# Performance work log

Hardware: AMD Instinct MI355X
Metric: run time of the kernel (lower is better)

The kernel has to match this reference:

```python
import jax, jax.numpy as jnp
import numpy as np

DIM = 24
HID = 256
N = 4096
NUM_LO = DIM * (DIM - 1) // 2  # 276
NEG = -0.01  # slope used in the hand-written Jacobians (source uses -0.01, NOT the fwd leaky slope 0.01; faithful)


def _linear_params(key, out_dim, in_dim):
    kw, kb = jax.random.split(key)
    s = 1.0 / np.sqrt(in_dim)
    W = jax.random.uniform(kw, (out_dim, in_dim), jnp.float32, -s, s)
    b = jax.random.uniform(kb, (out_dim,), jnp.float32, -s, s)
    return W, b


def setup_inputs() -> dict:
    key = jax.random.key(0)
    k = jax.random.split(key, 7)
    W1, b1 = _linear_params(k[0], HID, DIM)
    W2, b2 = _linear_params(k[1], HID, HID)
    WG, bG = _linear_params(k[2], DIM, HID)
    WLd, bLd = _linear_params(k[3], DIM, HID)
    WLo, bLo = _linear_params(k[4], NUM_LO, HID)
    q = jax.random.normal(k[5], (N, DIM), jnp.float32)
    q_dot = jax.random.normal(k[6], (N, DIM), jnp.float32)
    return {"q": q, "q_dot": q_dot, "W1": W1, "b1": b1, "W2": W2, "b2": b2,
            "WG": WG, "bG": bG, "WLd": WLd, "bLd": bLd, "WLo": WLo, "bLo": bLo}


def _forward(q, q_dot, W1, b1, W2, b2, WG, bG, WLd, bLd, WLo, bLo):
    n, d = q.shape
    tr, tc = np.tril_indices(d, -1)  # row-major strict-lower order == torch mask-flatten order
    di = np.arange(d)
    # MLP trunk (torch leaky_relu default slope 0.01)
    h1 = jax.nn.leaky_relu(q @ W1.T + b1)                       # [n,HID]
    h2 = jax.nn.leaky_relu(h1 @ W2.T + b2)                      # [n,HID]
    h3 = h2 @ WLd.T + bLd                                       # [n,d]
    g = h2 @ WG.T + bG                                          # [n,d]
    Ld = jax.nn.softplus(h3)                                    # [n,d]
    Lo = h2 @ WLo.T + bLo                                       # [n,NUM_LO]
    # Lower-triangular L (diag_embed(Ld) + masked strict-lower fill)
    L = jnp.zeros((n, d, d), q.dtype).at[:, tr, tc].set(Lo).at[:, di, di].set(Ld)
    # Hand-written Jacobian chain; diag_embed(v)@W == v[:,:,None]*W (direct elementwise scaling)
    dR1 = jnp.where(h1 > 0, 1.0, NEG)
    J1 = dR1[:, :, None] * W1                                    # dh1/dq  [n,HID,d]
    dR2 = jnp.where(h2 > 0, 1.0, NEG)
    J2 = dR2[:, :, None] * jnp.einsum('ij,njd->nid', W2, J1)     # dh2/dq  [n,HID,d]
    sig = jax.nn.sigmoid(h3)
    dld_dq = sig[:, :, None] * jnp.einsum('ij,njd->nid', WLd, J2)  # [n,d,d]
    dlo_dq = jnp.einsum('oj,njd->nod', WLo, J2)                  # [n,NUM_LO,d]
    dld_dt = jnp.einsum('nid,nd->ni', dld_dq, q_dot)             # [n,d]
    dlo_dt = jnp.einsum('nod,nd->no', dlo_dq, q_dot)             # [n,NUM_LO]
    dL_dt = jnp.zeros((n, d, d), q.dtype).at[:, tr, tc].set(dlo_dt).at[:, di, di].set(dld_dt)
    # 4D assembly: torch does L[L==1] = dlo_dq.view(-1), which reinterprets the (lo, q_idx)
    # flat buffer in (q_idx, tril_pos) order -> plain reshape replicates that exactly.
    vals = dlo_dq.reshape(n, d, NUM_LO)
    dld_dq_p = dld_dq.transpose(0, 2, 1)                         # [n, d_q, d_ld]
    dL_dq = jnp.zeros((n, d, d, d), q.dtype).at[:, :, tr, tc].set(vals).at[:, :, di, di].set(dld_dq_p)
    eye = jnp.eye(d, dtype=q.dtype)
    M = L @ L.transpose(0, 2, 1) + 1e-9 * eye
    dM_dt = L @ dL_dt.transpose(0, 2, 1) + dL_dt @ L.transpose(0, 2, 1)
    # Quadratic term. torch: q_dot.repeat(d,1)/L.repeat(d,1,1) index as (i % n) while
    # dL_dq.view(n*d,d,d) indexes as (i // d, i % d) -> replicate exactly (faithful).
    idx = jnp.arange(n * d) % n
    qd_r = q_dot[idx]                                            # [n*d, d]
    L_r = L[idx]                                                 # [n*d, d, d]
    dL_i = dL_dq.reshape(n * d, d, d)
    S = dL_i @ L_r.transpose(0, 2, 1) + L_r @ dL_i.transpose(0, 2, 1)
    quad = jnp.einsum('bi,bij,bj->b', qd_r, S, qd_r).reshape(n, d)
    c = jnp.einsum('nij,nj->ni', dM_dt, q_dot) - 0.5 * quad
    return M, c, g


def reference(q, q_dot, W1, b1, W2, b2, WG, bG, WLd, bLd, WLo, bLo):
    return _forward(q, q_dot, W1, b1, W2, b2, WG, bG, WLd, bLd, WLo, bLo)
```

## Files before the change

### kernel.cpp

```cpp
#include <hip/hip_runtime.h>
#include <math.h>

#define DIM 24
#define HID 256
#define NLO 276
#define NSAMP 4096
#define C_OFF 2359296
#define G_OFF 2457600

#define OFF_W2FH 0
#define OFF_W2FL 32768
#define OFF_WEFH 65536
#define OFF_WEFL 106496
#define OFF_W1H16 147456
#define OFF_W1L16 151552
#define OFF_W2H16 155648
#define OFF_W2L16 188416
#define OFF_WHH16 221184
#define OFF_WHL16 264192
#define OFF_MSKT 307200
#define OFF_SIGT 372736
#define OFF_LDT  471040
#define OFF_UT   569344
#define OFF_LOT  667648
#define OFF_W1PH 1798144
#define OFF_W1PL 1801216
#define OFF_W1NH 1804288
#define OFF_W1NL 1807360

typedef __attribute__((ext_vector_type(8))) short bf16x8;
typedef __attribute__((ext_vector_type(8))) _Float16 f16x8;
typedef __attribute__((ext_vector_type(4))) float f32x4;

__device__ __forceinline__ float leaky(float x){ return x > 0.f ? x : 0.01f*x; }
__device__ __forceinline__ unsigned short f2b(float f){
  unsigned u = __float_as_uint(f);
  return (unsigned short)((u + 0x7FFFu + ((u >> 16) & 1u)) >> 16);
}
__device__ __forceinline__ float b2f(unsigned short h){ return __uint_as_float(((unsigned)h) << 16); }
__device__ __forceinline__ void f2h2(float v, unsigned short* hi, unsigned short* lo){
  _Float16 h = (_Float16)v;
  _Float16 l = (_Float16)((v - (float)h) * 4096.f);
  *hi = *(unsigned short*)&h; *lo = *(unsigned short*)&l;
}

__global__ __launch_bounds__(256) void k0_prep(
    const float* __restrict__ W1, const float* __restrict__ W2,
    const float* __restrict__ WG, const float* __restrict__ WLd,
    const float* __restrict__ WLo, float* __restrict__ ws)
{
  const int tid = blockIdx.x*256 + threadIdx.x;
  const int nth = gridDim.x*256;
  unsigned short* W2FH = (unsigned short*)(ws + OFF_W2FH);
  unsigned short* W2FL = (unsigned short*)(ws + OFF_W2FL);
  for (int e = tid; e < 65536; e += nth){
    int j=e&7, l=(e>>3)&63, kb=(e>>9)&7, mt=e>>12;
    int m = mt*16+(l&15), k = kb*32+((l>>4)&3)*8+j;
    float v = W2[m*256+k];
    unsigned short h = f2b(v);
    W2FH[e]=h; W2FL[e]=f2b(v-b2f(h));
  }
  unsigned short* WEFH = (unsigned short*)(ws + OFF_WEFH);
  unsigned short* WEFL = (unsigned short*)(ws + OFF_WEFL);
  for (int e = tid; e < 81920; e += nth){
    int j=e&7, l=(e>>3)&63, kb=(e>>9)&7, mt=e>>12;
    int r = mt*16+(l&15), k = kb*32+((l>>4)&3)*8+j;
    float v = 0.f;
    if (r < 24) v = WLd[r*256+k]; else if (r < 300) v = WLo[(r-24)*256+k];
    unsigned short h = f2b(v);
    WEFH[e]=h; WEFL[e]=f2b(v-b2f(h));
  }
  unsigned short* W1H = (unsigned short*)(ws + OFF_W1H16);
  unsigned short* W1L = (unsigned short*)(ws + OFF_W1L16);
  for (int e = tid; e < 8192; e += nth){
    int j=e&7, l=(e>>3)&63, mt=e>>9;
    int m = mt*16+(l&15), k = ((l>>4)&3)*8+j;
    float v = (k < 24) ? W1[m*24+k] : 0.f;
    f2h2(v, &W1H[e], &W1L[e]);
  }
  unsigned short* W2H = (unsigned short*)(ws + OFF_W2H16);
  unsigned short* W2L = (unsigned short*)(ws + OFF_W2L16);
  for (int e = tid; e < 65536; e += nth){
    int j=e&7, l=(e>>3)&63, kb=(e>>9)&7, mt=e>>12;
    int m = mt*16+(l&15), k = kb*32+((l>>4)&3)*8+j;
    f2h2(W2[m*256+k], &W2H[e], &W2L[e]);
  }
  unsigned short* WHH = (unsigned short*)(ws + OFF_WHH16);
  unsigned short* WHL = (unsigned short*)(ws + OFF_WHL16);
  for (int e = tid; e < 86016; e += nth){
    int j=e&7, l=(e>>3)&63, kb=(e>>9)&7, mt=e>>12;
    int rr = mt*16+(l&15), k = kb*32+((l>>4)&3)*8+j;
    float v = 0.f;
    if (rr < 24) v = WLd[rr*256+k];
    else if (rr < 48) v = WG[(rr-24)*256+k];
    else if (rr < 324) v = WLo[(rr-48)*256+k];
    f2h2(v, &WHH[e], &WHL[e]);
  }
  unsigned short* W1PH = (unsigned short*)(ws + OFF_W1PH);
  unsigned short* W1PL = (unsigned short*)(ws + OFF_W1PL);
  unsigned short* W1NH = (unsigned short*)(ws + OFF_W1NH);
  unsigned short* W1NL = (unsigned short*)(ws + OFF_W1NL);
  for (int e = tid; e < 6144; e += nth){
    float v = W1[e];
    unsigned short h = f2b(v);
    W1PH[e] = h; W1PL[e] = f2b(v - b2f(h));
    float vn = -0.01f*v;
    unsigned short hn = f2b(vn);
    W1NH[e] = hn; W1NL[e] = f2b(vn - b2f(hn));
  }
}

__global__ __launch_bounds__(256) void k1_fwd(
    const float* __restrict__ q, const float* __restrict__ qd_g,
    const float* __restrict__ b1, const float* __restrict__ b2,
    const float* __restrict__ bG, const float* __restrict__ bLd,
    const float* __restrict__ bLo, float* __restrict__ ws,
    float* __restrict__ out)
{
  const int s0 = blockIdx.x*8, t = threadIdx.x;
  const int w = t>>6, l = t&63, l15 = l&15, l4g = (l>>4)&3;
  unsigned* MSKT = (unsigned*)(ws + OFF_MSKT);
  float* SIGT = ws + OFF_SIGT;
  float* LDT  = ws + OFF_LDT;
  float* UT   = ws + OFF_UT;
  float* LOT  = ws + OFF_LOT;

  __shared__ __align__(16) unsigned short pool[8448];
  __shared__ unsigned char mb[8][64];
  __shared__ float qd_s[8][24];
  __shared__ float Lsm[8][600];
  unsigned short* BQH = pool;
  unsigned short* BQL = BQH + 320;
  unsigned short* BH2 = pool;
  unsigned short* BL2 = BH2 + 2112;

  for (int f = t; f < 192; f += 256){
    float v = q[s0*24 + f];
    int n = f/24, k = f%24;
    f2h2(v, &BQH[n*40+k], &BQL[n*40+k]);
    ((float*)qd_s)[f] = qd_g[s0*24 + f];
  }
  if (t < 64){ int n = t>>3, k = 24 + (t&7); BQH[n*40+k]=0; BQL[n*40+k]=0; }
  __syncthreads();

  f32x4 aH[4], aX[4];
  #pragma unroll
  for (int i=0;i<4;++i){ aH[i]=(f32x4){0,0,0,0}; aX[i]=(f32x4){0,0,0,0}; }
  {
    const f16x8* WH = (const f16x8*)(ws + OFF_W1H16);
    const f16x8* WL = (const f16x8*)(ws + OFF_W1L16);
    f16x8 Af[4], Al[4];
    #pragma unroll
    for (int i=0;i<4;++i){ int mt=w+4*i; Af[i]=WH[mt*64+l]; Al[i]=WL[mt*64+l]; }
    int off = l15*40 + l4g*8;
    f16x8 Bh = *(const f16x8*)(BQH+off), Bl = *(const f16x8*)(BQL+off);
    #pragma unroll
    for (int i=0;i<4;++i){
      aH[i]=__builtin_amdgcn_mfma_f32_16x16x32_f16(Af[i],Bh,aH[i],0,0,0);
      aX[i]=__builtin_amdgcn_mfma_f32_16x16x32_f16(Af[i],Bl,aX[i],0,0,0);
      aX[i]=__builtin_amdgcn_mfma_f32_16x16x32_f16(Al[i],Bh,aX[i],0,0,0);
    }
  }
  __syncthreads();
  #pragma unroll
  for (int i=0;i<4;++i){
    int m0=(w+4*i)*16+4*l4g;
    float4 bb = *(const float4*)(b1+m0);
    int n = l15;
    if (n < 8){
      unsigned nib=0; unsigned short hs[4], ls[4];
      #pragma unroll
      for (int r=0;r<4;++r){
        float val = aH[i][r] + aX[i][r]*(1.f/4096.f) + ((const float*)&bb)[r];
        if (val > 0.f) nib |= 1u<<r;
        f2h2(leaky(val), &hs[r], &ls[r]);
      }
      mb[n][(m0>>2)] = (unsigned char)nib;
      *(uint2*)(BH2 + n*264 + m0) = make_uint2((unsigned)hs[0]|((unsigned)hs[1]<<16),
                                               (unsigned)hs[2]|((unsigned)hs[3]<<16));
      *(uint2*)(BL2 + n*264 + m0) = make_uint2((unsigned)ls[0]|((unsigned)ls[1]<<16),
                                               (unsigned)ls[2]|((unsigned)ls[3]<<16));
    }
  }
  __syncthreads();
  if (t < 64){
    int n = t&7, w8 = t>>3; unsigned word = 0;
    #pragma unroll
    for (int b=0;b<8;++b) word |= (unsigned)(mb[n][w8*8+b] & 0xFu) << (4*b);
    MSKT[w8*NSAMP + s0+n] = word;
  }

  #pragma unroll
  for (int i=0;i<4;++i){ aH[i]=(f32x4){0,0,0,0}; aX[i]=(f32x4){0,0,0,0}; }
  {
    const f16x8* WH = (const f16x8*)(ws + OFF_W2H16);
    const f16x8* WL = (const f16x8*)(ws + OFF_W2L16);
    for (int kb=0;kb<8;++kb){
      f16x8 Af[4], Al[4];
      #pragma unroll
      for (int i=0;i<4;++i){ int mt=w+4*i; Af[i]=WH[(mt*8+kb)*64+l]; Al[i]=WL[(mt*8+kb)*64+l]; }
      int off = l15*264 + kb*32 + l4g*8;
      f16x8 Bh = *(const f16x8*)(BH2+off), Bl = *(const f16x8*)(BL2+off);
      #pragma unroll
      for (int i=0;i<4;++i){
        aH[i]=__builtin_amdgcn_mfma_f32_16x16x32_f16(Af[i],Bh,aH[i],0,0,0);
        aX[i]=__builtin_amdgcn_mfma_f32_16x16x32_f16(Af[i],Bl,aX[i],0,0,0);
        aX[i]=__builtin_amdgcn_mfma_f32_16x16x32_f16(Al[i],Bh,aX[i],0,0,0);
      }
    }
  }
  __syncthreads();
  #pragma unroll
  for (int i=0;i<4;++i){
    int m0=(w+4*i)*16+4*l4g;
    float4 bb = *(const float4*)(b2+m0);
    int n = l15;
    if (n < 8){
      unsigned nib=0; unsigned short hs[4], ls[4];
      #pragma unroll
      for (int r=0;r<4;++r){
        float val = aH[i][r] + aX[i][r]*(1.f/4096.f) + ((const float*)&bb)[r];
        if (val > 0.f) nib |= 1u<<r;
        f2h2(leaky(val), &hs[r], &ls[r]);
      }
      mb[n][(m0>>2)] = (unsigned char)nib;
      *(uint2*)(BH2 + n*264 + m0) = make_uint2((unsigned)hs[0]|((unsigned)hs[1]<<16),
                                               (unsigned)hs[2]|((unsigned)hs[3]<<16));
      *(uint2*)(BL2 + n*264 + m0) = make_uint2((unsigned)ls[0]|((unsigned)ls[1]<<16),
                                               (unsigned)ls[2]|((unsigned)ls[3]<<16));
    }
  }
  __syncthreads();
  if (t < 64){
    int n = t&7, w8 = t>>3; unsigned word = 0;
    #pragma unroll
    for (int b=0;b<8;++b) word |= (unsigned)(mb[n][w8*8+b] & 0xFu) << (4*b);
    MSKT[(8+w8)*NSAMP + s0+n] = word;
  }

  for (int pass=0; pass<2; ++pass){
    f32x4 cH[3], cX[3];
    #pragma unroll
    for (int i=0;i<3;++i){ cH[i]=(f32x4){0,0,0,0}; cX[i]=(f32x4){0,0,0,0}; }
    const f16x8* WH = (const f16x8*)(ws + OFF_WHH16);
    const f16x8* WL = (const f16x8*)(ws + OFF_WHL16);
    for (int kb=0;kb<8;++kb){
      f16x8 Af[3], Al[3];
      #pragma unroll
      for (int i=0;i<3;++i){
        int mt = w + 4*(3*pass+i);
        if (mt < 21){ Af[i]=WH[(mt*8+kb)*64+l]; Al[i]=WL[(mt*8+kb)*64+l]; }
      }
      int off = l15*264 + kb*32 + l4g*8;
      f16x8 Bh = *(const f16x8*)(BH2+off), Bl = *(const f16x8*)(BL2+off);
      #pragma unroll
      for (int i=0;i<3;++i){
        int mt = w + 4*(3*pass+i);
        if (mt < 21){
          cH[i]=__builtin_amdgcn_mfma_f32_16x16x32_f16(Af[i],Bh,cH[i],0,0,0);
          cX[i]=__builtin_amdgcn_mfma_f32_16x16x32_f16(Af[i],Bl,cX[i],0,0,0);
          cX[i]=__builtin_amdgcn_mfma_f32_16x16x32_f16(Al[i],Bh,cX[i],0,0,0);
        }
      }
    }
    #pragma unroll
    for (int i=0;i<3;++i){
      int mt = w + 4*(3*pass+i);
      if (mt >= 21) continue;
      int m0 = mt*16+4*l4g;
      int n = l15;
      if (n < 8){
        int sG = s0+n;
        int tr = 0, tc = 0;
        if (m0 >= 48){
          int p = m0 - 48;
          tr = (int)((1.f + sqrtf(1.f + 8.f*(float)p))*0.5f);
          while (tr*(tr-1)/2 > p) --tr;
          while ((tr+1)*tr/2 <= p) ++tr;
          tc = p - tr*(tr-1)/2;
        }
        #pragma unroll
        for (int r=0;r<4;++r){
          int rr = m0+r;
          float val = cH[i][r] + cX[i][r]*(1.f/4096.f);
          if (rr < 24){
            val += bLd[rr];
            SIGT[rr*NSAMP + sG] = 1.f/(1.f + expf(-val));
            float sp = fmaxf(val,0.f) + log1pf(expf(-fabsf(val)));
            LDT[rr*NSAMP + sG] = sp;
            Lsm[n][rr*25 + rr] = sp;
          } else if (rr < 48){
            out[G_OFF + sG*24 + (rr-24)] = val + bG[rr-24];
          } else if (rr < 324){
            float lov = val + bLo[rr-48];
            LOT[(rr-48)*NSAMP + sG] = lov;
            Lsm[n][tr*25 + tc] = lov;
            if (++tc == tr){ ++tr; tc = 0; }
          }
        }
      }
    }
  }
  __syncthreads();

  for (int n2 = 0; n2 < 8; ++n2){
    const float* Ls = Lsm[n2];
    for (int e = t; e < 576; e += 256){
      int r = e/24, c = e%24, km = min(r,c);
      float acc = (r == c) ? 1e-9f : 0.f;
      for (int k = 0; k <= km; ++k) acc += Ls[r*25+k]*Ls[c*25+k];
      out[(size_t)(s0+n2)*576 + e] = acc;
    }
  }
  if (t < 192){
    int n = t/24, c = t%24;
    float u = qd_s[n][c]*Lsm[n][c*25+c];
    for (int r = c+1; r < 24; ++r) u += qd_s[n][r]*Lsm[n][r*25+c];
    UT[c*NSAMP + s0+n] = u;
  }
}

__global__ __launch_bounds__(256, 3) void kDE(
    const float* __restrict__ q_dot, float* __restrict__ ws, float* __restrict__ out)
{
  const int n0 = blockIdx.x*2, t = threadIdx.x;
  const int w = t >> 6, l = t & 63;
  const int l15 = l & 15, l4g = (l >> 4) & 3;
  const unsigned* MSKT = (const unsigned*)(ws + OFF_MSKT);
  const float* SIGT = ws + OFF_SIGT;
  const float* LDT  = ws + OFF_LDT;
  const float* UT   = ws + OFF_UT;
  const float* LOT  = ws + OFF_LOT;

  __shared__ __align__(16) char pool[50688];
  __shared__ unsigned msk[2][16];
  unsigned short* BH = (unsigned short*)pool;
  unsigned short* BL = BH + 12672;
  float* dlo_flat = (float*)pool;
  float* dld25    = (float*)(pool + 26496);
  float* qdm_s    = (float*)(pool + 28896);
  float* um_s     = (float*)(pool + 31296);
  float* qp2      = (float*)(pool + 33696);
  float* dtlo     = (float*)(pool + 40320);
  float* dtld     = (float*)(pool + 41424);
  float* w1s      = (float*)(pool + 41520);
  float* sigs     = (float*)(pool + 41616);
  float* qds      = (float*)(pool + 41712);
  float* uss      = (float*)(pool + 41808);
  float* qps      = (float*)(pool + 41904);

  if (t < 32) msk[t>>4][t&15] = MSKT[(t&15)*NSAMP + n0 + (t>>4)];
  __syncthreads();

  {
    bool p0 = (msk[0][t>>5] >> (t&31)) & 1u;
    bool p1 = (msk[1][t>>5] >> (t&31)) & 1u;
    const unsigned* h0 = (const unsigned*)((const unsigned short*)(ws + (p0 ? OFF_W1PH : OFF_W1NH)) + t*24);
    const unsigned* l0 = (const unsigned*)((const unsigned short*)(ws + (p0 ? OFF_W1PL : OFF_W1NL)) + t*24);
    const unsigned* h1 = (const unsigned*)((const unsigned short*)(ws + (p1 ? OFF_W1PH : OFF_W1NH)) + t*24);
    const unsigned* l1 = (const unsigned*)((const unsigned short*)(ws + (p1 ? OFF_W1PL : OFF_W1NL)) + t*24);
    #pragma unroll
    for (int j = 0; j < 12; ++j){
      unsigned dh0 = h0[j], dl0 = l0[j], dh1 = h1[j], dl1 = l1[j];
      BH[(2*j)*264 + t]      = (unsigned short)dh0;
      BH[(2*j+1)*264 + t]    = (unsigned short)(dh0 >> 16);
      BL[(2*j)*264 + t]      = (unsigned short)dl0;
      BL[(2*j+1)*264 + t]    = (unsigned short)(dl0 >> 16);
      BH[(24+2*j)*264 + t]   = (unsigned short)dh1;
      BH[(24+2*j+1)*264 + t] = (unsigned short)(dh1 >> 16);
      BL[(24+2*j)*264 + t]   = (unsigned short)dl1;
      BL[(24+2*j+1)*264 + t] = (unsigned short)(dl1 >> 16);
    }
  }
  __syncthreads();

  f32x4 accD[4][3];
  #pragma unroll
  for (int i = 0; i < 4; ++i)
    #pragma unroll
    for (int nt = 0; nt < 3; ++nt) accD[i][nt] = (f32x4){0.f,0.f,0.f,0.f};
  {
    const bf16x8* AHp = (const bf16x8*)(ws + OFF_W2FH);
    const bf16x8* ALp = (const bf16x8*)(ws + OFF_W2FL);
    for (int kb = 0; kb < 8; ++kb){
      bf16x8 AH[4], AL[4], BHf[3], BLf[3];
      #pragma unroll
      for (int i = 0; i < 4; ++i){
        int mt = 4*w + i;
        AH[i] = AHp[(mt*8+kb)*64 + l];
        AL[i] = ALp[(mt*8+kb)*64 + l];
      }
      #pragma unroll
      for (int nt = 0; nt < 3; ++nt){
        int off = (nt*16 + l15)*264 + kb*32 + l4g*8;
        BHf[nt] = *(const bf16x8*)(BH + off);
        BLf[nt] = *(const bf16x8*)(BL + off);
      }
      #pragma unroll
      for (int i = 0; i < 4; ++i)
        #pragma unroll
        for (int nt = 0; nt < 3; ++nt){
          accD[i][nt] = __builtin_amdgcn_mfma_f32_16x16x32_bf16(AH[i], BHf[nt], accD[i][nt], 0, 0, 0);
          accD[i][nt] = __builtin_amdgcn_mfma_f32_16x16x32_bf16(AH[i], BLf[nt], accD[i][nt], 0, 0, 0);
          accD[i][nt] = __builtin_amdgcn_mfma_f32_16x16x32_bf16(AL[i], BHf[nt], accD[i][nt], 0, 0, 0);
        }
    }
  }
  __syncthreads();

  #pragma unroll
  for (int i = 0; i < 4; ++i){
    int mt = 4*w + i;
    int m0 = mt*16 + 4*l4g;
    int bb = m0 & 31;
    #pragma unroll
    for (int nt = 0; nt < 3; ++nt){
      int c = nt*16 + l15;
      int s = c >= 24;
      unsigned word = msk[s][8 + (mt>>1)];
      unsigned uh[4], ul[4];
      #pragma unroll
      for (int r = 0; r < 4; ++r){
        float sc = ((word >> (bb + r)) & 1u) ? 1.f : -0.01f;
        float v = sc * accD[i][nt][r];
        unsigned uv = __float_as_uint(v);
        uh[r] = uv;
        float lo = v - __uint_as_float(uv & 0xFFFF0000u);
        ul[r] = __float_as_uint(lo);
      }
      *(uint2*)(BH + c*264 + m0) = make_uint2((uh[0]>>16) | (uh[1] & 0xFFFF0000u),
                                              (uh[2]>>16) | (uh[3] & 0xFFFF0000u));
      *(uint2*)(BL + c*264 + m0) = make_uint2((ul[0]>>16) | (ul[1] & 0xFFFF0000u),
                                              (ul[2]>>16) | (ul[3] & 0xFFFF0000u));
    }
  }
  __syncthreads();

  f32x4 accE[5][3];
  #pragma unroll
  for (int i = 0; i < 5; ++i)
    #pragma unroll
    for (int nt = 0; nt < 3; ++nt) accE[i][nt] = (f32x4){0.f,0.f,0.f,0.f};
  {
    const bf16x8* AHp = (const bf16x8*)(ws + OFF_WEFH);
    const bf16x8* ALp = (const bf16x8*)(ws + OFF_WEFL);
    for (int kb = 0; kb < 8; ++kb){
      bf16x8 AH[5], AL[5], BHf[3], BLf[3];
      #pragma unroll
      for (int i = 0; i < 5; ++i){
        int mt = 5*w + i;
        AH[i] = AHp[(mt*8+kb)*64 + l];
        AL[i] = ALp[(mt*8+kb)*64 + l];
      }
      #pragma unroll
      for (int nt = 0; nt < 3; ++nt){
        int off = (nt*16 + l15)*264 + kb*32 + l4g*8;
        BHf[nt] = *(const bf16x8*)(BH + off);
        BLf[nt] = *(const bf16x8*)(BL + off);
      }
      #pragma unroll
      for (int i = 0; i < 5; ++i)
        #pragma unroll
        for (int nt = 0; nt < 3; ++nt){
          accE[i][nt] = __builtin_amdgcn_mfma_f32_16x16x32_bf16(AH[i], BHf[nt], accE[i][nt], 0, 0, 0);
          accE[i][nt] = __builtin_amdgcn_mfma_f32_16x16x32_bf16(AH[i], BLf[nt], accE[i][nt], 0, 0, 0);
          accE[i][nt] = __builtin_amdgcn_mfma_f32_16x16x32_bf16(AL[i], BHf[nt], accE[i][nt], 0, 0, 0);
        }
    }
  }
  __syncthreads();

  for (int s = 0; s < 2; ++s){
    const int n = n0 + s;
    #pragma unroll
    for (int i = 0; i < 5; ++i){
      int mt = 5*w + i;
      #pragma unroll
      for (int nt = 0; nt < 3; ++nt){
        int c = nt*16 + l15;
        if ((c >= 24) == (s == 1)){
          int d = c - 24*s;
          #pragma unroll
          for (int r = 0; r < 4; ++r){
            int re = mt*16 + 4*l4g + r;
            if (re < 24) dld25[re*25 + d] = accE[i][nt][r];
            else if (re < 300) dlo_flat[(re-24)*24 + d] = accE[i][nt][r];
          }
        }
      }
    }
    for (int e = t; e < 576; e += 256){
      int a_ = e/24, b_ = e%24;
      int ma = (n*24 + a_) & (NSAMP-1);
      int mb_ = (n*24 + b_) & (NSAMP-1);
      qdm_s[a_*25 + b_] = q_dot[ma*24 + b_];
      um_s[a_*25 + b_]  = UT[a_*NSAMP + mb_];
    }
    if (t < 24){
      sigs[t] = SIGT[t*NSAMP + n];
      qds[t]  = q_dot[n*24 + t];
      uss[t]  = UT[t*NSAMP + n];
    }
    __syncthreads();

    for (int k = t; k < 1656; k += 256){
      float4 v = *(const float4*)(dlo_flat + 4*k);
      int j4 = (k % 6)*4;
      qp2[k] = v.x*qds[j4] + v.y*qds[j4+1] + v.z*qds[j4+2] + v.w*qds[j4+3];
    }
    if (t < 24){
      float a = 0.f;
      #pragma unroll
      for (int d = 0; d < 24; ++d) a += dld25[t*25+d]*qds[d];
      dtld[t] = sigs[t]*a;
    }
    __syncthreads();

    for (int o = t; o < 276; o += 256){
      float a = 0.f;
      #pragma unroll
      for (int j = 0; j < 6; ++j) a += qp2[o*6+j];
      dtlo[o] = a;
    }
    __syncthreads();

    if (t < 96){
      int g = t/24, i = t%24;
      float part = 0.f;
      for (int c2 = g; c2 < 24; c2 += 4){
        float v = qdm_s[i*25+c2]*sigs[c2]*dld25[c2*25+i];
        for (int r = c2+1; r < 24; ++r){
          int p = r*(r-1)/2 + c2;
          v += qdm_s[i*25+r]*dlo_flat[i*276 + p];
        }
        part += um_s[c2*25+i]*v;
      }
      qps[g*24 + i] = part;
    } else if (t >= 128 && t < 152){
      int i = t - 128;
      float a = qds[i]*dtld[i];
      for (int j = i+1; j < 24; ++j) a += qds[j]*dtlo[j*(j-1)/2 + i];
      w1s[i] = a;
    }
    __syncthreads();

    if (t < 24){
      const int i = t;
      float cs = dtld[i]*uss[i] + LDT[i*NSAMP + n]*w1s[i];
      for (int k = 0; k < i; ++k){
        int p = i*(i-1)/2 + k;
        cs += LOT[p*NSAMP + n]*w1s[k] + dtlo[p]*uss[k];
      }
      float quad = qps[i] + qps[24+i] + qps[48+i] + qps[72+i];
      out[C_OFF + n*24 + i] = cs - quad;
    }
    __syncthreads();
  }
}

extern "C" void kernel_launch(void* const* d_in, const int* in_sizes, int n_in,
                              void* d_out, int out_size, void* d_ws, size_t ws_size,
                              hipStream_t stream)
{
  const float* q   = (const float*)d_in[0];
  const float* qd  = (const float*)d_in[1];
  const float* W1  = (const float*)d_in[2];
  const float* b1  = (const float*)d_in[3];
  const float* W2  = (const float*)d_in[4];
  const float* b2  = (const float*)d_in[5];
  const float* WG  = (const float*)d_in[6];
  const float* bG  = (const float*)d_in[7];
  const float* WLd = (const float*)d_in[8];
  const float* bLd = (const float*)d_in[9];
  const float* WLo = (const float*)d_in[10];
  const float* bLo = (const float*)d_in[11];
  float* out = (float*)d_out;
  float* ws  = (float*)d_ws;

  k0_prep<<<256, 256, 0, stream>>>(W1, W2, WG, WLd, WLo, ws);
  k1_fwd<<<NSAMP/8, 256, 0, stream>>>(q, qd, b1, b2, bG, bLd, bLo, ws, out);
  kDE<<<NSAMP/2, 256, 0, stream>>>(qd, ws, out);
}
```

Measured before the change: 254.4 us.

## Halve samples per forward block and build W1 Jacobian tiles on the fly

The forward kernel now handles 4 samples per block instead of 8 and launches twice as many blocks, so more CUs have work during the MLP stage. Each MFMA tile is 16 columns wide, so fewer of its columns now carry real samples and weights are reloaded per block more often. The prep kernel no longer precomputes sign-scaled bf16 hi/lo copies of W1. Instead the Jacobian kernel reads W1 directly, scales it by the activation-slope mask and splits it into bf16 hi/lo in registers. This drops a workspace pass but adds conversion arithmetic to every Jacobian block.

```diff
diff --git a/kernel.cpp b/kernel.cpp
--- a/kernel.cpp
+++ b/kernel.cpp
@@ -23,10 +23,6 @@
 #define OFF_LDT  471040
 #define OFF_UT   569344
 #define OFF_LOT  667648
-#define OFF_W1PH 1798144
-#define OFF_W1PL 1801216
-#define OFF_W1NH 1804288
-#define OFF_W1NL 1807360
 
 typedef __attribute__((ext_vector_type(8))) short bf16x8;
 typedef __attribute__((ext_vector_type(8))) _Float16 f16x8;
@@ -96,18 +92,6 @@
     else if (rr < 324) v = WLo[(rr-48)*256+k];
     f2h2(v, &WHH[e], &WHL[e]);
   }
-  unsigned short* W1PH = (unsigned short*)(ws + OFF_W1PH);
-  unsigned short* W1PL = (unsigned short*)(ws + OFF_W1PL);
-  unsigned short* W1NH = (unsigned short*)(ws + OFF_W1NH);
-  unsigned short* W1NL = (unsigned short*)(ws + OFF_W1NL);
-  for (int e = tid; e < 6144; e += nth){
-    float v = W1[e];
-    unsigned short h = f2b(v);
-    W1PH[e] = h; W1PL[e] = f2b(v - b2f(h));
-    float vn = -0.01f*v;
-    unsigned short hn = f2b(vn);
-    W1NH[e] = hn; W1NL[e] = f2b(vn - b2f(hn));
-  }
 }
 
 __global__ __launch_bounds__(256) void k1_fwd(
@@ -117,7 +101,7 @@
     const float* __restrict__ bLo, float* __restrict__ ws,
     float* __restrict__ out)
 {
-  const int s0 = blockIdx.x*8, t = threadIdx.x;
+  const int s0 = blockIdx.x*4, t = threadIdx.x;
   const int w = t>>6, l = t&63, l15 = l&15, l4g = (l>>4)&3;
   unsigned* MSKT = (unsigned*)(ws + OFF_MSKT);
   float* SIGT = ws + OFF_SIGT;
@@ -126,21 +110,21 @@
   float* LOT  = ws + OFF_LOT;
 
   __shared__ __align__(16) unsigned short pool[8448];
-  __shared__ unsigned char mb[8][64];
-  __shared__ float qd_s[8][24];
-  __shared__ float Lsm[8][600];
+  __shared__ unsigned char mb[4][64];
+  __shared__ float qd_s[4][24];
+  __shared__ float Lsm[4][600];
   unsigned short* BQH = pool;
-  unsigned short* BQL = BQH + 320;
+  unsigned short* BQL = BQH + 160;
   unsigned short* BH2 = pool;
-  unsigned short* BL2 = BH2 + 2112;
-
-  for (int f = t; f < 192; f += 256){
+  unsigned short* BL2 = BH2 + 4224;
+
+  for (int f = t; f < 96; f += 256){
     float v = q[s0*24 + f];
     int n = f/24, k = f%24;
     f2h2(v, &BQH[n*40+k], &BQL[n*40+k]);
     ((float*)qd_s)[f] = qd_g[s0*24 + f];
   }
-  if (t < 64){ int n = t>>3, k = 24 + (t&7); BQH[n*40+k]=0; BQL[n*40+k]=0; }
+  if (t < 32){ int n = t>>3, k = 24 + (t&7); BQH[n*40+k]=0; BQL[n*40+k]=0; }
   __syncthreads();
 
   f32x4 aH[4], aX[4];
@@ -167,7 +151,7 @@
     int m0=(w+4*i)*16+4*l4g;
     float4 bb = *(const float4*)(b1+m0);
     int n = l15;
-    if (n < 8){
+    if (n < 4){
       unsigned nib=0; unsigned short hs[4], ls[4];
       #pragma unroll
       for (int r=0;r<4;++r){
@@ -183,8 +167,8 @@
     }
   }
   __syncthreads();
-  if (t < 64){
-    int n = t&7, w8 = t>>3; unsigned word = 0;
+  if (t < 32){
+    int n = t&3, w8 = t>>2; unsigned word = 0;
     #pragma unroll
     for (int b=0;b<8;++b) word |= (unsigned)(mb[n][w8*8+b] & 0xFu) << (4*b);
     MSKT[w8*NSAMP + s0+n] = word;
@@ -215,7 +199,7 @@
     int m0=(w+4*i)*16+4*l4g;
     float4 bb = *(const float4*)(b2+m0);
     int n = l15;
-    if (n < 8){
+    if (n < 4){
       unsigned nib=0; unsigned short hs[4], ls[4];
       #pragma unroll
       for (int r=0;r<4;++r){
@@ -231,8 +215,8 @@
     }
   }
   __syncthreads();
-  if (t < 64){
-    int n = t&7, w8 = t>>3; unsigned word = 0;
+  if (t < 32){
+    int n = t&3, w8 = t>>2; unsigned word = 0;
     #pragma unroll
     for (int b=0;b<8;++b) word |= (unsigned)(mb[n][w8*8+b] & 0xFu) << (4*b);
     MSKT[(8+w8)*NSAMP + s0+n] = word;
@@ -269,7 +253,7 @@
       if (mt >= 21) continue;
       int m0 = mt*16+4*l4g;
       int n = l15;
-      if (n < 8){
+      if (n < 4){
         int sG = s0+n;
         int tr = 0, tc = 0;
         if (m0 >= 48){
@@ -303,7 +287,7 @@
   }
   __syncthreads();
 
-  for (int n2 = 0; n2 < 8; ++n2){
+  for (int n2 = 0; n2 < 4; ++n2){
     const float* Ls = Lsm[n2];
     for (int e = t; e < 576; e += 256){
       int r = e/24, c = e%24, km = min(r,c);
@@ -312,7 +296,7 @@
       out[(size_t)(s0+n2)*576 + e] = acc;
     }
   }
-  if (t < 192){
+  if (t < 96){
     int n = t/24, c = t%24;
     float u = qd_s[n][c]*Lsm[n][c*25+c];
     for (int r = c+1; r < 24; ++r) u += qd_s[n][r]*Lsm[n][r*25+c];
@@ -321,7 +305,8 @@
 }
 
 __global__ __launch_bounds__(256, 3) void kDE(
-    const float* __restrict__ q_dot, float* __restrict__ ws, float* __restrict__ out)
+    const float* __restrict__ q_dot, const float* __restrict__ W1g,
+    float* __restrict__ ws, float* __restrict__ out)
 {
   const int n0 = blockIdx.x*2, t = threadIdx.x;
   const int w = t >> 6, l = t & 63;
@@ -353,23 +338,18 @@
   __syncthreads();
 
   {
-    bool p0 = (msk[0][t>>5] >> (t&31)) & 1u;
-    bool p1 = (msk[1][t>>5] >> (t&31)) & 1u;
-    const unsigned* h0 = (const unsigned*)((const unsigned short*)(ws + (p0 ? OFF_W1PH : OFF_W1NH)) + t*24);
-    const unsigned* l0 = (const unsigned*)((const unsigned short*)(ws + (p0 ? OFF_W1PL : OFF_W1NL)) + t*24);
-    const unsigned* h1 = (const unsigned*)((const unsigned short*)(ws + (p1 ? OFF_W1PH : OFF_W1NH)) + t*24);
-    const unsigned* l1 = (const unsigned*)((const unsigned short*)(ws + (p1 ? OFF_W1PL : OFF_W1NL)) + t*24);
-    #pragma unroll
-    for (int j = 0; j < 12; ++j){
-      unsigned dh0 = h0[j], dl0 = l0[j], dh1 = h1[j], dl1 = l1[j];
-      BH[(2*j)*264 + t]      = (unsigned short)dh0;
-      BH[(2*j+1)*264 + t]    = (unsigned short)(dh0 >> 16);
-      BL[(2*j)*264 + t]      = (unsigned short)dl0;
-      BL[(2*j+1)*264 + t]    = (unsigned short)(dl0 >> 16);
-      BH[(24+2*j)*264 + t]   = (unsigned short)dh1;
-      BH[(24+2*j+1)*264 + t] = (unsigned short)(dh1 >> 16);
-      BL[(24+2*j)*264 + t]   = (unsigned short)dl1;
-      BL[(24+2*j+1)*264 + t] = (unsigned short)(dl1 >> 16);
+    float w1r[24];
+    #pragma unroll
+    for (int d = 0; d < 24; ++d) w1r[d] = W1g[t*24 + d];
+    float dr0 = ((msk[0][t>>5] >> (t&31)) & 1u) ? 1.f : -0.01f;
+    float dr1 = ((msk[1][t>>5] >> (t&31)) & 1u) ? 1.f : -0.01f;
+    #pragma unroll
+    for (int c = 0; c < 48; ++c){
+      int s = c >= 24, d = c - 24*s;
+      float f = (s ? dr1 : dr0) * w1r[d];
+      unsigned short h = f2b(f);
+      BH[c*264 + t] = h;
+      BL[c*264 + t] = f2b(f - b2f(h));
     }
   }
   __syncthreads();
@@ -578,6 +558,6 @@
   float* ws  = (float*)d_ws;
 
   k0_prep<<<256, 256, 0, stream>>>(W1, W2, WG, WLd, WLo, ws);
-  k1_fwd<<<NSAMP/8, 256, 0, stream>>>(q, qd, b1, b2, bG, bLd, bLo, ws, out);
-  kDE<<<NSAMP/2, 256, 0, stream>>>(qd, ws, out);
+  k1_fwd<<<NSAMP/4, 256, 0, stream>>>(q, qd, b1, b2, bG, bLd, bLo, ws, out);
+  kDE<<<NSAMP/2, 256, 0, stream>>>(qd, W1, ws, out);
 }
```

Result: slower. 281.4 us (+10.6%).
